# Kernel tuning notes

Hardware: AMD Instinct MI355X
Metric: run time of the kernel (lower is better)

Reference implementation:

```python
import jax, jax.numpy as jnp
import numpy as np

B, S, D_MODEL, D_K, D_V = 4, 2048, 1024, 1024, 1024


def setup_inputs() -> dict:
    key = jax.random.key(0)
    k1, k2, k3, k4 = jax.random.split(key, 4)
    scale = 1.0 / np.sqrt(D_MODEL)
    x = jax.random.normal(k1, (B, S, D_MODEL), dtype=jnp.float32)
    Wq = jax.random.normal(k2, (D_K, D_MODEL), dtype=jnp.float32) * scale
    Wk = jax.random.normal(k3, (D_K, D_MODEL), dtype=jnp.float32) * scale
    Wv = jax.random.normal(k4, (D_V, D_MODEL), dtype=jnp.float32) * scale
    # causal mask: position i may attend to j <= i (True = keep)
    mask = jnp.broadcast_to(jnp.tril(jnp.ones((S, S), dtype=bool)), (B, S, S))
    return {"x": x, "mask": mask, "Wq": Wq, "Wk": Wk, "Wv": Wv}


def reference(x, mask, Wq, Wk, Wv):
    # nn.Linear(d, k, bias=False): y = x @ W.T with W of shape [k, d]
    q = jnp.einsum('bsd,kd->bsk', x, Wq)
    k = jnp.einsum('bsd,kd->bsk', x, Wk)
    v = jnp.einsum('bsd,vd->bsv', x, Wv)
    scores = jnp.einsum('bik,bjk->bij', q, k) / jnp.sqrt(jnp.float32(D_K))
    s = jnp.where(mask, scores, -jnp.inf)
    # masked, fully-masked-row-safe softmax (fully masked rows -> all zeros,
    # matching softmax[all-masked rows] = 0 in the original)
    m = jnp.max(s, axis=-1, keepdims=True)
    m_safe = jnp.where(jnp.isfinite(m), m, 0.0)
    e = jnp.exp(s - m_safe)          # exp(-inf) = 0 for masked entries
    denom = jnp.sum(e, axis=-1, keepdims=True)
    p = e / jnp.where(denom == 0.0, 1.0, denom)
    return jnp.einsum('bij,bjv->biv', p, v)
```

## Files before the change

kernel.cpp:

```cpp
#include <hip/hip_runtime.h>
#include <hip/hip_bf16.h>
#include <stdint.h>

#define SEQ   2048
#define DM    1024
#define NBAT  4

typedef __attribute__((ext_vector_type(8))) short  short8;
typedef __attribute__((ext_vector_type(4))) float  floatx4;

__device__ __forceinline__ unsigned short f2b(float f) {
    __hip_bfloat16 h = __float2bfloat16(f);
    unsigned short r;
    __builtin_memcpy(&r, &h, 2);
    return r;
}

__device__ __forceinline__ ushort4 pack4(float a, float b, float c, float d) {
    ushort4 u; u.x = f2b(a); u.y = f2b(b); u.z = f2b(c); u.w = f2b(d); return u;
}

__device__ __forceinline__ void gload16(const void* g, void* s) {
    __builtin_amdgcn_global_load_lds(
        (const __attribute__((address_space(1))) unsigned int*)(uintptr_t)g,
        (__attribute__((address_space(3))) unsigned int*)(uintptr_t)s,
        16, 0, 0);
}

__global__ void prep(const float4* __restrict__ x,
                     const float4* __restrict__ w0, const float4* __restrict__ w1,
                     const float4* __restrict__ w2,
                     ushort4* __restrict__ xb, ushort4* __restrict__ wall,
                     float* __restrict__ rsum)
{
    const int b = blockIdx.x;
    const int t = threadIdx.x;
    if (b < 8192) {
        const int i = b * 256 + t;
        float4 f = x[i];
        xb[i] = pack4(f.x, f.y, f.z, f.w);
    } else if (b < 11264) {
        const int idx  = b - 8192;
        const int wsel = idx >> 10;
        const int i    = (idx & 1023) * 256 + t;
        const float4* src = (wsel == 0) ? w0 : (wsel == 1) ? w1 : w2;
        float4 f = src[i];
        wall[(size_t)wsel * 262144 + i] = pack4(f.x, f.y, f.z, f.w);
    } else {
        rsum[(b - 11264) * 256 + t] = 0.f;
    }
}

__global__ __launch_bounds__(256) void qkv_gemm(
    const unsigned short* __restrict__ A, const unsigned short* __restrict__ Bm,
    unsigned short* __restrict__ Qo, unsigned short* __restrict__ Ko,
    unsigned short* __restrict__ Vto, float qscale)
{
    const int m0 = blockIdx.y * 128;
    const int n0 = blockIdx.x * 128;
    const int K  = DM;

    __shared__ __align__(16) unsigned short As[128 * 64];
    __shared__ __align__(16) unsigned short Bs[128 * 64];

    const int t    = threadIdx.x;
    const int w    = t >> 6;
    const int lane = t & 63;
    const int wr   = w >> 1, wc = w & 1;
    const int r    = lane & 15, q = lane >> 4;

    floatx4 acc[4][4];
#pragma unroll
    for (int i = 0; i < 4; i++)
#pragma unroll
        for (int j = 0; j < 4; j++)
            acc[i][j] = (floatx4){0.f, 0.f, 0.f, 0.f};

    const int rr0 = t >> 3;
    const int pg  = (t & 7) ^ ((t >> 3) & 7);
    const int swz = r & 7;

    for (int k0 = 0; k0 < K; k0 += 64) {
        const size_t ka = (size_t)k0 + pg * 8;
#pragma unroll
        for (int g = 0; g < 4; g++) {
            gload16(A  + (size_t)(m0 + g * 32 + rr0) * K + ka, As + g * 2048 + (size_t)w * 512);
            gload16(Bm + (size_t)(n0 + g * 32 + rr0) * K + ka, Bs + g * 2048 + (size_t)w * 512);
        }
        __builtin_amdgcn_s_waitcnt(0);
        __syncthreads();

#pragma unroll
        for (int kk = 0; kk < 2; kk++) {
            short8 af[4], bf[4];
            const int slot = ((kk * 4 + q) ^ swz) * 8;
#pragma unroll
            for (int i = 0; i < 4; i++) {
                af[i] = *(const short8*)&As[(wr * 64 + i * 16 + r) * 64 + slot];
                bf[i] = *(const short8*)&Bs[(wc * 64 + i * 16 + r) * 64 + slot];
            }
#pragma unroll
            for (int i = 0; i < 4; i++)
#pragma unroll
                for (int j = 0; j < 4; j++)
                    acc[i][j] = __builtin_amdgcn_mfma_f32_16x16x32_bf16(af[i], bf[j], acc[i][j], 0, 0, 0);
        }
        __syncthreads();
    }

    const int gmb = m0 + wr * 64 + q * 4;
    const int gnb = n0 + wc * 64 + r;
#pragma unroll
    for (int i = 0; i < 4; i++) {
        const int gm = gmb + i * 16;
#pragma unroll
        for (int j = 0; j < 4; j++) {
            const int gn = gnb + j * 16;
            if (n0 < 1024) {
#pragma unroll
                for (int rr = 0; rr < 4; rr++)
                    Qo[(size_t)(gm + rr) * 1024 + gn] = f2b(acc[i][j][rr] * qscale);
            } else if (n0 < 2048) {
#pragma unroll
                for (int rr = 0; rr < 4; rr++)
                    Ko[(size_t)(gm + rr) * 1024 + (gn - 1024)] = f2b(acc[i][j][rr]);
            } else {
                const int b = gm >> 11;
                const int s = gm & 2047;
                const int v = gn - 2048;
                *(ushort4*)&Vto[((size_t)(b * 1024 + v)) * 2048 + s] =
                    pack4(acc[i][j][0], acc[i][j][1], acc[i][j][2], acc[i][j][3]);
            }
        }
    }
}

template<int MODE>
__global__ __launch_bounds__(256) void attn64(
    const unsigned short* __restrict__ Ag, const unsigned short* __restrict__ Bg,
    void* __restrict__ Cv, float* __restrict__ rowsum)
{
    const int z = blockIdx.z;
    int m0, n0;
    if (MODE == 0) {
        const int f = blockIdx.x;
        int ti = (int)((sqrtf(4.f * f + 1.f) - 1.f) * 0.5f);
        while ((ti + 1) * (ti + 2) <= f) ti++;
        while (ti * (ti + 1) > f) ti--;
        const int tj = f - ti * (ti + 1);
        m0 = ti * 128;
        n0 = tj * 64;
    } else {
        m0 = (int)(gridDim.y - 1 - blockIdx.y) * 128;
        n0 = blockIdx.x * 64;
    }

    const int lda = (MODE == 0) ? DM : SEQ;
    const int ldb = (MODE == 0) ? DM : SEQ;
    const unsigned short* A  = Ag + (size_t)z * ((MODE == 0) ? SEQ * DM : SEQ * SEQ);
    const unsigned short* Bm = Bg + (size_t)z * ((MODE == 0) ? SEQ * DM : DM * SEQ);
    const int kEnd = (MODE == 0) ? DM : (m0 + 128);

    __shared__ __align__(16) unsigned short As[128 * 64];
    __shared__ __align__(16) unsigned short Bs[64 * 64];

    const int t    = threadIdx.x;
    const int w    = t >> 6;
    const int lane = t & 63;
    const int r    = lane & 15, q = lane >> 4;

    floatx4 acc[2][4];
#pragma unroll
    for (int i = 0; i < 2; i++)
#pragma unroll
        for (int j = 0; j < 4; j++)
            acc[i][j] = (floatx4){0.f, 0.f, 0.f, 0.f};

    const int rr0 = t >> 3;
    const int pg  = (t & 7) ^ ((t >> 3) & 7);
    const int swz = r & 7;

    for (int k0 = 0; k0 < kEnd; k0 += 64) {
        const size_t ka = (size_t)k0 + pg * 8;
#pragma unroll
        for (int g = 0; g < 4; g++)
            gload16(A + (size_t)(m0 + g * 32 + rr0) * lda + ka,
                    As + g * 2048 + (size_t)w * 512);
#pragma unroll
        for (int g = 0; g < 2; g++)
            gload16(Bm + (size_t)(n0 + g * 32 + rr0) * ldb + ka,
                    Bs + g * 2048 + (size_t)w * 512);
        __builtin_amdgcn_s_waitcnt(0);
        __syncthreads();

#pragma unroll
        for (int kk = 0; kk < 2; kk++) {
            short8 af[2], bf[4];
            const int slot = ((kk * 4 + q) ^ swz) * 8;
#pragma unroll
            for (int i = 0; i < 2; i++)
                af[i] = *(const short8*)&As[(w * 32 + i * 16 + r) * 64 + slot];
#pragma unroll
            for (int j = 0; j < 4; j++)
                bf[j] = *(const short8*)&Bs[(j * 16 + r) * 64 + slot];
#pragma unroll
            for (int i = 0; i < 2; i++)
#pragma unroll
                for (int j = 0; j < 4; j++)
                    acc[i][j] = __builtin_amdgcn_mfma_f32_16x16x32_bf16(bf[j], af[i], acc[i][j], 0, 0, 0);
        }
        __syncthreads();
    }

    const int gmb = m0 + w * 32 + r;
    const int gnb = n0 + q * 4;
    if (MODE == 0) {
        unsigned short* E = (unsigned short*)Cv + (size_t)z * SEQ * SEQ;
        float* rs = rowsum + (size_t)z * SEQ;
#pragma unroll
        for (int i = 0; i < 2; i++) {
            const int gm = gmb + i * 16;
            float part = 0.f;
#pragma unroll
            for (int j = 0; j < 4; j++) {
                const int gn = gnb + j * 16;
                float e0 = (gn + 0 <= gm) ? __expf(acc[i][j][0]) : 0.f;
                float e1 = (gn + 1 <= gm) ? __expf(acc[i][j][1]) : 0.f;
                float e2 = (gn + 2 <= gm) ? __expf(acc[i][j][2]) : 0.f;
                float e3 = (gn + 3 <= gm) ? __expf(acc[i][j][3]) : 0.f;
                part += (e0 + e1) + (e2 + e3);
                *(ushort4*)&E[(size_t)gm * SEQ + gn] = pack4(e0, e1, e2, e3);
            }
            part += __shfl_xor(part, 16, 64);
            part += __shfl_xor(part, 32, 64);
            if (q == 0) atomicAdd(&rs[gm], part);
        }
    } else {
        float* C = (float*)Cv + (size_t)z * SEQ * DM;
        const float* rs = rowsum + (size_t)z * SEQ;
#pragma unroll
        for (int i = 0; i < 2; i++) {
            const int gm = gmb + i * 16;
            const float inv = 1.0f / rs[gm];
#pragma unroll
            for (int j = 0; j < 4; j++) {
                const int gn = gnb + j * 16;
                float4 o;
                o.x = acc[i][j][0] * inv;
                o.y = acc[i][j][1] * inv;
                o.z = acc[i][j][2] * inv;
                o.w = acc[i][j][3] * inv;
                *(float4*)&C[(size_t)gm * DM + gn] = o;
            }
        }
    }
}

extern "C" void kernel_launch(void* const* d_in, const int* in_sizes, int n_in,
                              void* d_out, int out_size, void* d_ws, size_t ws_size,
                              hipStream_t stream) {
    (void)in_sizes; (void)n_in; (void)out_size; (void)ws_size;
    const float* x  = (const float*)d_in[0];
    const float* Wq = (const float*)d_in[2];
    const float* Wk = (const float*)d_in[3];
    const float* Wv = (const float*)d_in[4];

    char* base = (char*)d_ws;
    size_t off = 0;
    auto alloc = [&](size_t n) { char* p = base + off; off += (n + 255) & ~(size_t)255; return p; };

    unsigned short* xb   = (unsigned short*)alloc((size_t)NBAT * SEQ * DM * 2);
    unsigned short* wall = (unsigned short*)alloc((size_t)3 * DM * DM * 2);
    unsigned short* Qb   = (unsigned short*)alloc((size_t)NBAT * SEQ * DM * 2);
    unsigned short* Kb   = (unsigned short*)alloc((size_t)NBAT * SEQ * DM * 2);
    unsigned short* Vtb  = (unsigned short*)alloc((size_t)NBAT * DM * SEQ * 2);
    unsigned short* E    = (unsigned short*)alloc((size_t)NBAT * SEQ * SEQ * 2);
    float*          rsum = (float*)alloc((size_t)NBAT * SEQ * 4);

    const dim3 blk(256);

    prep<<<dim3(11296), blk, 0, stream>>>(
        (const float4*)x, (const float4*)Wq, (const float4*)Wk, (const float4*)Wv,
        (ushort4*)xb, (ushort4*)wall, rsum);

    const int Mtot = NBAT * SEQ;

    qkv_gemm<<<dim3(3 * DM / 128, Mtot / 128, 1), blk, 0, stream>>>(
        xb, wall, Qb, Kb, Vtb, 0.03125f);

    attn64<0><<<dim3(272, 1, NBAT), blk, 0, stream>>>(Qb, Kb, E, rsum);

    attn64<1><<<dim3(DM / 64, SEQ / 128, NBAT), blk, 0, stream>>>(E, Vtb, d_out, rsum);
}
```

Baseline: 280.2 us.

## Shrink QKV GEMM k-tile to 32, pair triangular tiles in attention block mapping

The QKV GEMM now stages 32-wide k slices instead of 64, which halves LDS use per block but doubles the number of barrier and wait rounds and removes the XOR swizzle on the LDS layout. The attention kernels replace the sqrt-based triangular index decode and the reversed row order with a mapping that interleaves row tiles p and 15-p across consecutive block indices. This balances causal work among neighbouring blocks and makes the decode cheap. The PV kernel becomes a 1-D grid of 256 blocks per batch using that mapping.

```diff
diff --git a/kernel.cpp b/kernel.cpp
--- a/kernel.cpp
+++ b/kernel.cpp
@@ -60,8 +60,8 @@
     const int n0 = blockIdx.x * 128;
     const int K  = DM;
 
-    __shared__ __align__(16) unsigned short As[128 * 64];
-    __shared__ __align__(16) unsigned short Bs[128 * 64];
+    __shared__ __align__(16) unsigned short As[128 * 32];
+    __shared__ __align__(16) unsigned short Bs[128 * 32];
 
     const int t    = threadIdx.x;
     const int w    = t >> 6;
@@ -76,35 +76,29 @@
         for (int j = 0; j < 4; j++)
             acc[i][j] = (floatx4){0.f, 0.f, 0.f, 0.f};
 
-    const int rr0 = t >> 3;
-    const int pg  = (t & 7) ^ ((t >> 3) & 7);
-    const int swz = r & 7;
-
-    for (int k0 = 0; k0 < K; k0 += 64) {
-        const size_t ka = (size_t)k0 + pg * 8;
-#pragma unroll
-        for (int g = 0; g < 4; g++) {
-            gload16(A  + (size_t)(m0 + g * 32 + rr0) * K + ka, As + g * 2048 + (size_t)w * 512);
-            gload16(Bm + (size_t)(n0 + g * 32 + rr0) * K + ka, Bs + g * 2048 + (size_t)w * 512);
-        }
+    const int row0 = t >> 2;
+    const int cc0  = t & 3;
+
+    for (int k0 = 0; k0 < K; k0 += 32) {
+        const size_t ka = (size_t)k0 + cc0 * 8;
+        gload16(A  + (size_t)(m0 + row0)      * K + ka, As + (size_t)w * 512);
+        gload16(A  + (size_t)(m0 + row0 + 64) * K + ka, As + 2048 + (size_t)w * 512);
+        gload16(Bm + (size_t)(n0 + row0)      * K + ka, Bs + (size_t)w * 512);
+        gload16(Bm + (size_t)(n0 + row0 + 64) * K + ka, Bs + 2048 + (size_t)w * 512);
         __builtin_amdgcn_s_waitcnt(0);
         __syncthreads();
 
-#pragma unroll
-        for (int kk = 0; kk < 2; kk++) {
-            short8 af[4], bf[4];
-            const int slot = ((kk * 4 + q) ^ swz) * 8;
-#pragma unroll
-            for (int i = 0; i < 4; i++) {
-                af[i] = *(const short8*)&As[(wr * 64 + i * 16 + r) * 64 + slot];
-                bf[i] = *(const short8*)&Bs[(wc * 64 + i * 16 + r) * 64 + slot];
-            }
-#pragma unroll
-            for (int i = 0; i < 4; i++)
-#pragma unroll
-                for (int j = 0; j < 4; j++)
-                    acc[i][j] = __builtin_amdgcn_mfma_f32_16x16x32_bf16(af[i], bf[j], acc[i][j], 0, 0, 0);
-        }
+        short8 af[4], bf[4];
+#pragma unroll
+        for (int i = 0; i < 4; i++) {
+            af[i] = *(const short8*)&As[(wr * 64 + i * 16 + r) * 32 + q * 8];
+            bf[i] = *(const short8*)&Bs[(wc * 64 + i * 16 + r) * 32 + q * 8];
+        }
+#pragma unroll
+        for (int i = 0; i < 4; i++)
+#pragma unroll
+            for (int j = 0; j < 4; j++)
+                acc[i][j] = __builtin_amdgcn_mfma_f32_16x16x32_bf16(af[i], bf[j], acc[i][j], 0, 0, 0);
         __syncthreads();
     }
 
@@ -144,15 +138,22 @@
     int m0, n0;
     if (MODE == 0) {
         const int f = blockIdx.x;
-        int ti = (int)((sqrtf(4.f * f + 1.f) - 1.f) * 0.5f);
-        while ((ti + 1) * (ti + 2) <= f) ti++;
-        while (ti * (ti + 1) > f) ti--;
-        const int tj = f - ti * (ti + 1);
+        const int p = f & 7;
+        const int k = f >> 3;
+        int ti, tj;
+        if (k < 2 * p + 2) { ti = p;      tj = k; }
+        else               { ti = 15 - p; tj = k - (2 * p + 2); }
         m0 = ti * 128;
         n0 = tj * 64;
     } else {
-        m0 = (int)(gridDim.y - 1 - blockIdx.y) * 128;
-        n0 = blockIdx.x * 64;
+        const int f = blockIdx.x;
+        const int p = f & 7;
+        const int k = f >> 3;
+        int ti, nt;
+        if (k < 16) { ti = p;      nt = k; }
+        else        { ti = 15 - p; nt = k - 16; }
+        m0 = ti * 128;
+        n0 = nt * 64;
     }
 
     const int lda = (MODE == 0) ? DM : SEQ;
@@ -290,5 +291,5 @@
 
     attn64<0><<<dim3(272, 1, NBAT), blk, 0, stream>>>(Qb, Kb, E, rsum);
 
-    attn64<1><<<dim3(DM / 64, SEQ / 128, NBAT), blk, 0, stream>>>(E, Vtb, d_out, rsum);
-}
+    attn64<1><<<dim3(256, 1, NBAT), blk, 0, stream>>>(E, Vtb, d_out, rsum);
+}
```

After: 289.1 us. 3.2% more time.
